# Optimization experiments

Hardware: AMD Instinct MI355X
Metric: run time of the kernel (lower is better)

## Reference

```python
import jax, jax.numpy as jnp
import numpy as np

N = 30000      # nodes
E = 480000     # edges (before self-loops)
F_IN = 128     # dim_in
H = 8          # heads
C = 32         # dim_h (per-head channels)
F_H = H * C    # concat hidden width = 256
NEG_SLOPE = 0.2


def setup_inputs() -> dict:
    key = jax.random.key(0)
    ks = jax.random.split(key, 12)
    def glorot(k, shape, fan):
        return jax.random.normal(k, shape, jnp.float32) * (1.0 / np.sqrt(fan))
    return {
        "x": jax.random.normal(ks[0], (N, F_IN), jnp.float32),
        "edge_index": jax.random.randint(ks[1], (2, E), 0, N),
        "W1": glorot(ks[2], (F_IN, F_H), F_IN),
        "a1_src": glorot(ks[3], (H, C), C),
        "a1_dst": glorot(ks[4], (H, C), C),
        "b1": jnp.zeros((F_H,), jnp.float32),
        "W2": glorot(ks[5], (F_H, F_H), F_H),
        "a2_src": glorot(ks[6], (H, C), C),
        "a2_dst": glorot(ks[7], (H, C), C),
        "b2": jnp.zeros((F_H,), jnp.float32),
        "Wl": glorot(ks[8], (F_H, 1), F_H),
        "bl": jnp.zeros((1,), jnp.float32),
    }


def gat_conv(x, src, dst, W, a_src, a_dst, b):
    """PyG-style GATConv (concat=True, add_self_loops handled by caller)."""
    n = x.shape[0]
    h = (x @ W).reshape(n, H, C)                       # [N,H,C]
    alpha_s = jnp.einsum('nhc,hc->nh', h, a_src)        # [N,H]
    alpha_d = jnp.einsum('nhc,hc->nh', h, a_dst)        # [N,H]
    e = jax.nn.leaky_relu(alpha_s[src] + alpha_d[dst], NEG_SLOPE)  # [E,H]
    # segment softmax over incoming edges of each destination node
    e_max = jax.ops.segment_max(e, dst, num_segments=n)            # [N,H]
    e_max = jnp.where(jnp.isfinite(e_max), e_max, 0.0)
    e_exp = jnp.exp(e - e_max[dst])                                # [E,H]
    denom = jax.ops.segment_sum(e_exp, dst, num_segments=n)        # [N,H]
    alpha = e_exp / (denom[dst] + 1e-16)                           # [E,H]
    out = jax.ops.segment_sum(h[src] * alpha[:, :, None], dst, num_segments=n)  # [N,H,C]
    return out.reshape(n, F_H) + b


def reference(x, edge_index, W1, a1_src, a1_dst, b1, W2, a2_src, a2_dst, b2, Wl, bl):
    loops = jnp.arange(N, dtype=edge_index.dtype)      # self-loops (PyG default)
    src = jnp.concatenate([edge_index[0], loops])
    dst = jnp.concatenate([edge_index[1], loops])
    h = jax.nn.elu(gat_conv(x, src, dst, W1, a1_src, a1_dst, b1))
    h = jax.nn.elu(gat_conv(h, src, dst, W2, a2_src, a2_dst, b2))
    return (h @ Wl + bl).squeeze(1)                    # [N]
```

## Files before the change

kernel.cpp:

```cpp
#include <hip/hip_runtime.h>
#include <hip/hip_bf16.h>

#define NNODES 30000
#define NEDGES 480000
#define TE (NEDGES + NNODES)
#define FH 256
#define NH 8
#define NSB ((NNODES + 255) / 256)

typedef unsigned short ushort_t;
typedef __attribute__((ext_vector_type(8))) _Float16 f16x8;
typedef __attribute__((ext_vector_type(2))) _Float16 f16x2;
typedef __attribute__((ext_vector_type(4))) float f32x4;

__global__ void zero_counts(int* __restrict__ c) {
    int i = blockIdx.x * 256 + threadIdx.x;
    if (i < NNODES) c[i] = 0;
}

__global__ void count_kernel(const int* __restrict__ ei, int* __restrict__ counts) {
    int e = blockIdx.x * 256 + threadIdx.x;
    if (e >= TE) return;
    int d = (e < NEDGES) ? ei[NEDGES + e] : (e - NEDGES);
    atomicAdd(&counts[d], 1);
}

__global__ __launch_bounds__(256) void scan1_kernel(const int* __restrict__ counts,
                                                    int* __restrict__ rp,
                                                    int* __restrict__ bsum) {
    __shared__ int s[256];
    const int tid = threadIdx.x;
    const int i = blockIdx.x * 256 + tid;
    int v = (i < NNODES) ? counts[i] : 0;
    s[tid] = v;
    __syncthreads();
    for (int off = 1; off < 256; off <<= 1) {
        int t = (tid >= off) ? s[tid - off] : 0;
        __syncthreads();
        s[tid] += t;
        __syncthreads();
    }
    if (i < NNODES) rp[i] = s[tid] - v;
    if (tid == 255) bsum[blockIdx.x] = s[255];
}

__global__ __launch_bounds__(128) void scan2_kernel(int* __restrict__ bsum) {
    __shared__ int s[128];
    const int tid = threadIdx.x;
    int v = (tid < NSB) ? bsum[tid] : 0;
    s[tid] = v;
    __syncthreads();
    for (int off = 1; off < 128; off <<= 1) {
        int t = (tid >= off) ? s[tid - off] : 0;
        __syncthreads();
        s[tid] += t;
        __syncthreads();
    }
    if (tid < NSB) bsum[tid] = s[tid] - v;
}

__global__ __launch_bounds__(256) void scan3_kernel(int* __restrict__ rp,
                                                    const int* __restrict__ bsum,
                                                    int* __restrict__ cursor) {
    const int i = blockIdx.x * 256 + threadIdx.x;
    if (i < NNODES) {
        int r = rp[i] + bsum[blockIdx.x];
        rp[i] = r;
        cursor[i] = r;
    }
    if (i == 0) rp[NNODES] = TE;
}

__global__ void fill_kernel(const int* __restrict__ ei, int* __restrict__ cursor,
                            int* __restrict__ ssrc) {
    int e = blockIdx.x * 256 + threadIdx.x;
    if (e >= TE) return;
    int s, d;
    if (e < NEDGES) { s = ei[e]; d = ei[NEDGES + e]; }
    else            { s = e - NEDGES; d = s; }
    int pos = atomicAdd(&cursor[d], 1);
    ssrc[pos] = s;
}

__device__ __forceinline__ unsigned f2h2(float a, float b) {
    f16x2 h;
    h.x = (_Float16)a;
    h.y = (_Float16)b;
    return __builtin_bit_cast(unsigned, h);
}

__global__ void cvtT_w_both(const float* __restrict__ W1, const float* __restrict__ W2,
                            _Float16* __restrict__ t1, _Float16* __restrict__ t2) {
    int idx = blockIdx.x * 256 + threadIdx.x;
    if (idx < 128 * 256) {
        int n = idx & 255, k = idx >> 8;
        t1[n * 128 + k] = (_Float16)W1[idx];
    }
    int j = idx - 128 * 256;
    if (j >= 0 && j < 256 * 256) {
        int n = j & 255, k = j >> 8;
        t2[n * 256 + k] = (_Float16)W2[j];
    }
}

template<int K, bool CVT>
__global__ __launch_bounds__(512) void gemm_mfma(
    const void* __restrict__ Araw,  const _Float16* __restrict__ Bt,
    const float* __restrict__ ASRC, const float* __restrict__ ADST,
    _Float16* __restrict__ HFh, float* __restrict__ AS, float* __restrict__ AD) {

    constexpr int LDK = 40;
    __shared__ _Float16 Ah[128][LDK];
    __shared__ _Float16 Bh[256][LDK];

    const int tid  = threadIdx.x;
    const int lane = tid & 63;
    const int wid  = tid >> 6;
    const int m0 = blockIdx.x * 128;
    const int wm = (wid & 1) * 64;
    const int wn = (wid >> 1) * 64;
    const int q = lane >> 4;
    const int c = lane & 15;

    f32x4 acc[4][4];
#pragma unroll
    for (int mi = 0; mi < 4; ++mi)
#pragma unroll
        for (int ni = 0; ni < 4; ++ni) acc[mi][ni] = (f32x4){0.f, 0.f, 0.f, 0.f};

    for (int k0 = 0; k0 < K; k0 += 32) {
        __syncthreads();
        {
            int row = tid >> 2;
            int ch  = (tid & 3) * 8;
            int gr = m0 + row;
            uint4 v = make_uint4(0u, 0u, 0u, 0u);
            if (gr < NNODES) {
                if (CVT) {
                    const float* Xf = (const float*)Araw;
                    float4 f0 = *reinterpret_cast<const float4*>(&Xf[(size_t)gr * K + k0 + ch]);
                    float4 f1 = *reinterpret_cast<const float4*>(&Xf[(size_t)gr * K + k0 + ch + 4]);
                    v.x = f2h2(f0.x, f0.y); v.y = f2h2(f0.z, f0.w);
                    v.z = f2h2(f1.x, f1.y); v.w = f2h2(f1.z, f1.w);
                } else {
                    const _Float16* Ah_g = (const _Float16*)Araw;
                    v = *reinterpret_cast<const uint4*>(&Ah_g[(size_t)gr * K + k0 + ch]);
                }
            }
            *reinterpret_cast<uint4*>(&Ah[row][ch]) = v;
        }
#pragma unroll
        for (int rep = 0; rep < 2; ++rep) {
            int idx = tid + 512 * rep;
            int row = idx >> 2;
            int ch  = (idx & 3) * 8;
            uint4 bv = *reinterpret_cast<const uint4*>(&Bt[(size_t)row * K + k0 + ch]);
            *reinterpret_cast<uint4*>(&Bh[row][ch]) = bv;
        }
        __syncthreads();

        const int koff = q * 8;
        f16x8 fa[4], fb[4];
#pragma unroll
        for (int mi = 0; mi < 4; ++mi)
            fa[mi] = *reinterpret_cast<const f16x8*>(&Ah[wm + mi * 16 + c][koff]);
#pragma unroll
        for (int ni = 0; ni < 4; ++ni)
            fb[ni] = *reinterpret_cast<const f16x8*>(&Bh[wn + ni * 16 + c][koff]);
#pragma unroll
        for (int mi = 0; mi < 4; ++mi)
#pragma unroll
            for (int ni = 0; ni < 4; ++ni)
                acc[mi][ni] = __builtin_amdgcn_mfma_f32_16x16x32_f16(fa[mi], fb[ni], acc[mi][ni], 0, 0, 0);
    }

    float as_v[4], ad_v[4];
#pragma unroll
    for (int ni = 0; ni < 4; ++ni) {
        as_v[ni] = ASRC[wn + ni * 16 + c];
        ad_v[ni] = ADST[wn + ni * 16 + c];
    }
    const int head0 = wn >> 5;

#pragma unroll
    for (int mi = 0; mi < 4; ++mi) {
#pragma unroll
        for (int j = 0; j < 4; ++j) {
            int row = m0 + wm + mi * 16 + q * 4 + j;
            bool ok = row < NNODES;
            if (ok) {
#pragma unroll
                for (int ni = 0; ni < 4; ++ni)
                    HFh[(size_t)row * FH + wn + ni * 16 + c] = (_Float16)acc[mi][ni][j];
            }
            float ps0 = acc[mi][0][j] * as_v[0] + acc[mi][1][j] * as_v[1];
            float ps1 = acc[mi][2][j] * as_v[2] + acc[mi][3][j] * as_v[3];
            float pd0 = acc[mi][0][j] * ad_v[0] + acc[mi][1][j] * ad_v[1];
            float pd1 = acc[mi][2][j] * ad_v[2] + acc[mi][3][j] * ad_v[3];
#pragma unroll
            for (int off = 8; off >= 1; off >>= 1) {
                ps0 += __shfl_xor(ps0, off);
                ps1 += __shfl_xor(ps1, off);
                pd0 += __shfl_xor(pd0, off);
                pd1 += __shfl_xor(pd1, off);
            }
            if (ok && c == 0) {
                AS[row * NH + head0]     = ps0;
                AS[row * NH + head0 + 1] = ps1;
                AD[row * NH + head0]     = pd0;
                AD[row * NH + head0 + 1] = pd1;
            }
        }
    }
}

template<bool FINAL>
__global__ __launch_bounds__(256) void aggregate(
    const _Float16* __restrict__ HFh,
    const float* __restrict__ AS, const float* __restrict__ AD,
    const int* __restrict__ rp, const int* __restrict__ ssrc,
    const float* __restrict__ BIAS,
    _Float16* __restrict__ X2H,
    const float* __restrict__ WL, const float* __restrict__ BL,
    float* __restrict__ OUT) {

    __shared__ float wslab[4][64 * 10];

    const int tid  = threadIdx.x;
    const int lane = tid & 63;
    const int wid  = tid >> 6;
    const int node = __builtin_amdgcn_readfirstlane(blockIdx.x * 4 + wid);
    const int epar = lane >> 5;
    const int cg   = lane & 31;
    const int hh   = cg >> 2;
    const int c8   = cg * 8;
    float* wl = wslab[wid];

    const int p0  = rp[node];
    const int deg = rp[node + 1] - p0;

    const float4 ad0 = *reinterpret_cast<const float4*>(&AD[node * NH]);
    const float4 ad1 = *reinterpret_cast<const float4*>(&AD[node * NH + 4]);

    float a0=0.f,a1=0.f,a2=0.f,a3=0.f,a4=0.f,a5=0.f,a6=0.f,a7=0.f;
    float den = 0.f;

    for (int base = 0; base < deg; base += 64) {
        const int ne = min(64, deg - base);

        if (lane < ne) {
            int s = ssrc[p0 + base + lane];
            float4 as0 = *reinterpret_cast<const float4*>(&AS[s * NH]);
            float4 as1 = *reinterpret_cast<const float4*>(&AS[s * NH + 4]);
            float sv[8] = {as0.x + ad0.x, as0.y + ad0.y, as0.z + ad0.z, as0.w + ad0.w,
                           as1.x + ad1.x, as1.y + ad1.y, as1.z + ad1.z, as1.w + ad1.w};
            float* wp = &wl[lane * 10];
#pragma unroll
            for (int h = 0; h < 8; ++h) {
                float t = sv[h] > 0.f ? sv[h] : 0.2f * sv[h];
                wp[h] = __expf(t);
            }
            wp[8] = __int_as_float(s);
        }
        asm volatile("s_waitcnt lgkmcnt(0)" ::: "memory");

#pragma unroll 4
        for (int e0 = 0; e0 < ne; e0 += 2) {
            const int  e   = e0 + epar;
            const bool act = e < ne;
            const int  ee  = act ? e : 0;
            const int  sa  = __float_as_int(wl[ee * 10 + 8]);
            const float wr = wl[ee * 10 + hh];
            const float w  = act ? wr : 0.f;
            den += w;
            const f16x8 hv = *reinterpret_cast<const f16x8*>(&HFh[(size_t)sa * FH + c8]);
            a0 = fmaf((float)hv[0], w, a0);
            a1 = fmaf((float)hv[1], w, a1);
            a2 = fmaf((float)hv[2], w, a2);
            a3 = fmaf((float)hv[3], w, a3);
            a4 = fmaf((float)hv[4], w, a4);
            a5 = fmaf((float)hv[5], w, a5);
            a6 = fmaf((float)hv[6], w, a6);
            a7 = fmaf((float)hv[7], w, a7);
        }
    }

    a0 += __shfl_xor(a0, 32); a1 += __shfl_xor(a1, 32);
    a2 += __shfl_xor(a2, 32); a3 += __shfl_xor(a3, 32);
    a4 += __shfl_xor(a4, 32); a5 += __shfl_xor(a5, 32);
    a6 += __shfl_xor(a6, 32); a7 += __shfl_xor(a7, 32);
    den += __shfl_xor(den, 32);

    const float inv = 1.f / (den + 1e-16f);
    const float4 b0 = *reinterpret_cast<const float4*>(&BIAS[c8]);
    const float4 b1 = *reinterpret_cast<const float4*>(&BIAS[c8 + 4]);
    float o[8];
    o[0] = fmaf(a0, inv, b0.x); o[1] = fmaf(a1, inv, b0.y);
    o[2] = fmaf(a2, inv, b0.z); o[3] = fmaf(a3, inv, b0.w);
    o[4] = fmaf(a4, inv, b1.x); o[5] = fmaf(a5, inv, b1.y);
    o[6] = fmaf(a6, inv, b1.z); o[7] = fmaf(a7, inv, b1.w);
#pragma unroll
    for (int j = 0; j < 8; ++j) o[j] = o[j] > 0.f ? o[j] : expm1f(o[j]);

    if (!FINAL) {
        uint2 st;
        st.x = f2h2(o[epar * 4 + 0], o[epar * 4 + 1]);
        st.y = f2h2(o[epar * 4 + 2], o[epar * 4 + 3]);
        *reinterpret_cast<uint2*>(&X2H[(size_t)node * FH + c8 + epar * 4]) = st;
    } else {
        const float4 w0 = *reinterpret_cast<const float4*>(&WL[c8]);
        const float4 w1 = *reinterpret_cast<const float4*>(&WL[c8 + 4]);
        float pl = fmaf(o[0], w0.x, fmaf(o[1], w0.y, fmaf(o[2], w0.z, o[3] * w0.w)));
        pl = fmaf(o[4], w1.x, fmaf(o[5], w1.y, fmaf(o[6], w1.z, fmaf(o[7], w1.w, pl))));
#pragma unroll
        for (int off = 16; off >= 1; off >>= 1) pl += __shfl_xor(pl, off);
        if (lane == 0) OUT[node] = pl + BL[0];
    }
}

extern "C" void kernel_launch(void* const* d_in, const int* in_sizes, int n_in,
                              void* d_out, int out_size, void* d_ws, size_t ws_size,
                              hipStream_t stream) {
    const float* x   = (const float*)d_in[0];
    const int*   ei  = (const int*)d_in[1];
    const float* W1  = (const float*)d_in[2];
    const float* a1s = (const float*)d_in[3];
    const float* a1d = (const float*)d_in[4];
    const float* b1  = (const float*)d_in[5];
    const float* W2  = (const float*)d_in[6];
    const float* a2s = (const float*)d_in[7];
    const float* a2d = (const float*)d_in[8];
    const float* b2  = (const float*)d_in[9];
    const float* Wl  = (const float*)d_in[10];
    const float* bl  = (const float*)d_in[11];
    float* out = (float*)d_out;

    char* w = (char*)d_ws;
    auto alloc = [&](size_t bytes) -> char* {
        char* p = w;
        w += (bytes + 255) & ~size_t(255);
        return p;
    };
    int*   counts = (int*)alloc((size_t)NNODES * 4);
    int*   rp     = (int*)alloc((size_t)(NNODES + 1) * 4);
    int*   cursor = (int*)alloc((size_t)NNODES * 4);
    int*   bsum   = (int*)alloc((size_t)NSB * 4);
    int*   ssrc   = (int*)alloc((size_t)TE * 4);
    _Float16* hfh = (_Float16*)alloc((size_t)NNODES * FH * 2);
    _Float16* x2h = (_Float16*)alloc((size_t)NNODES * FH * 2);
    float* asb    = (float*)alloc((size_t)NNODES * NH * 4);
    float* adb    = (float*)alloc((size_t)NNODES * NH * 4);
    _Float16* w1t = (_Float16*)alloc((size_t)128 * 256 * 2);
    _Float16* w2t = (_Float16*)alloc((size_t)256 * 256 * 2);

    zero_counts<<<NSB, 256, 0, stream>>>(counts);
    count_kernel<<<(TE + 255) / 256, 256, 0, stream>>>(ei, counts);
    scan1_kernel<<<NSB, 256, 0, stream>>>(counts, rp, bsum);
    scan2_kernel<<<1, 128, 0, stream>>>(bsum);
    scan3_kernel<<<NSB, 256, 0, stream>>>(rp, bsum, cursor);
    fill_kernel<<<(TE + 255) / 256, 256, 0, stream>>>(ei, cursor, ssrc);

    cvtT_w_both<<<(128 * 256 + 256 * 256 + 255) / 256, 256, 0, stream>>>(W1, W2, w1t, w2t);

    const int gblocks = (NNODES + 127) / 128;
    gemm_mfma<128, true><<<gblocks, 512, 0, stream>>>(x, w1t, a1s, a1d, hfh, asb, adb);
    aggregate<false><<<NNODES / 4, 256, 0, stream>>>(hfh, asb, adb, rp, ssrc, b1,
                                                     x2h, nullptr, nullptr, nullptr);
    gemm_mfma<256, false><<<gblocks, 512, 0, stream>>>(x2h, w2t, a2s, a2d, hfh, asb, adb);
    aggregate<true><<<NNODES / 4, 256, 0, stream>>>(hfh, asb, adb, rp, ssrc, b2,
                                                    nullptr, Wl, bl, out);
}
```

Before: 179.5 us.

## Fuse CSR build into one persistent kernel with software grid barriers

Replaces the six CSR-construction launches (zero, count, three scan stages, fill) and the weight conversion launch with two kernels. A prep kernel zeroes counts and barrier counters and transposes the weights, and a persistent 120-block CSR kernel performs count, scan and fill, separated by atomic spin grid barriers. This is meant to remove launch overhead and inter-kernel gaps, in exchange for relying on all 120 blocks being co-resident and running the count and fill phases on far fewer threads.

```diff
diff --git a/kernel.cpp b/kernel.cpp
--- a/kernel.cpp
+++ b/kernel.cpp
@@ -6,81 +6,13 @@
 #define TE (NEDGES + NNODES)
 #define FH 256
 #define NH 8
-#define NSB ((NNODES + 255) / 256)
+#define CSRB 120
+#define CHUNK 250
 
 typedef unsigned short ushort_t;
 typedef __attribute__((ext_vector_type(8))) _Float16 f16x8;
 typedef __attribute__((ext_vector_type(2))) _Float16 f16x2;
 typedef __attribute__((ext_vector_type(4))) float f32x4;
-
-__global__ void zero_counts(int* __restrict__ c) {
-    int i = blockIdx.x * 256 + threadIdx.x;
-    if (i < NNODES) c[i] = 0;
-}
-
-__global__ void count_kernel(const int* __restrict__ ei, int* __restrict__ counts) {
-    int e = blockIdx.x * 256 + threadIdx.x;
-    if (e >= TE) return;
-    int d = (e < NEDGES) ? ei[NEDGES + e] : (e - NEDGES);
-    atomicAdd(&counts[d], 1);
-}
-
-__global__ __launch_bounds__(256) void scan1_kernel(const int* __restrict__ counts,
-                                                    int* __restrict__ rp,
-                                                    int* __restrict__ bsum) {
-    __shared__ int s[256];
-    const int tid = threadIdx.x;
-    const int i = blockIdx.x * 256 + tid;
-    int v = (i < NNODES) ? counts[i] : 0;
-    s[tid] = v;
-    __syncthreads();
-    for (int off = 1; off < 256; off <<= 1) {
-        int t = (tid >= off) ? s[tid - off] : 0;
-        __syncthreads();
-        s[tid] += t;
-        __syncthreads();
-    }
-    if (i < NNODES) rp[i] = s[tid] - v;
-    if (tid == 255) bsum[blockIdx.x] = s[255];
-}
-
-__global__ __launch_bounds__(128) void scan2_kernel(int* __restrict__ bsum) {
-    __shared__ int s[128];
-    const int tid = threadIdx.x;
-    int v = (tid < NSB) ? bsum[tid] : 0;
-    s[tid] = v;
-    __syncthreads();
-    for (int off = 1; off < 128; off <<= 1) {
-        int t = (tid >= off) ? s[tid - off] : 0;
-        __syncthreads();
-        s[tid] += t;
-        __syncthreads();
-    }
-    if (tid < NSB) bsum[tid] = s[tid] - v;
-}
-
-__global__ __launch_bounds__(256) void scan3_kernel(int* __restrict__ rp,
-                                                    const int* __restrict__ bsum,
-                                                    int* __restrict__ cursor) {
-    const int i = blockIdx.x * 256 + threadIdx.x;
-    if (i < NNODES) {
-        int r = rp[i] + bsum[blockIdx.x];
-        rp[i] = r;
-        cursor[i] = r;
-    }
-    if (i == 0) rp[NNODES] = TE;
-}
-
-__global__ void fill_kernel(const int* __restrict__ ei, int* __restrict__ cursor,
-                            int* __restrict__ ssrc) {
-    int e = blockIdx.x * 256 + threadIdx.x;
-    if (e >= TE) return;
-    int s, d;
-    if (e < NEDGES) { s = ei[e]; d = ei[NEDGES + e]; }
-    else            { s = e - NEDGES; d = s; }
-    int pos = atomicAdd(&cursor[d], 1);
-    ssrc[pos] = s;
-}
 
 __device__ __forceinline__ unsigned f2h2(float a, float b) {
     f16x2 h;
@@ -89,17 +21,94 @@
     return __builtin_bit_cast(unsigned, h);
 }
 
-__global__ void cvtT_w_both(const float* __restrict__ W1, const float* __restrict__ W2,
-                            _Float16* __restrict__ t1, _Float16* __restrict__ t2) {
-    int idx = blockIdx.x * 256 + threadIdx.x;
-    if (idx < 128 * 256) {
-        int n = idx & 255, k = idx >> 8;
-        t1[n * 128 + k] = (_Float16)W1[idx];
-    }
-    int j = idx - 128 * 256;
+__global__ __launch_bounds__(256) void prep_kernel(
+    int* __restrict__ counts, int* __restrict__ bar,
+    const float* __restrict__ W1, const float* __restrict__ W2,
+    _Float16* __restrict__ t1, _Float16* __restrict__ t2) {
+    int i = blockIdx.x * 256 + threadIdx.x;
+    if (i < NNODES) counts[i] = 0;
+    if (i < 8) bar[i] = 0;
+    if (i < 128 * 256) {
+        int n = i & 255, k = i >> 8;
+        t1[n * 128 + k] = (_Float16)W1[i];
+    }
+    int j = i - 128 * 256;
     if (j >= 0 && j < 256 * 256) {
         int n = j & 255, k = j >> 8;
         t2[n * 256 + k] = (_Float16)W2[j];
+    }
+}
+
+__device__ __forceinline__ void gridbar(int* __restrict__ bar, int phase, int tid) {
+    __syncthreads();
+    if (tid == 0) {
+        __threadfence();
+        atomicAdd(&bar[phase], 1);
+        while (__hip_atomic_load(&bar[phase], __ATOMIC_ACQUIRE,
+                                 __HIP_MEMORY_SCOPE_AGENT) < CSRB) { }
+    }
+    __syncthreads();
+}
+
+__global__ __launch_bounds__(256) void csr_kernel(
+    const int* __restrict__ ei, int* __restrict__ counts,
+    int* __restrict__ rp, int* __restrict__ cursor, int* __restrict__ ssrc,
+    int* __restrict__ bar, int* __restrict__ bsum) {
+
+    __shared__ int s[256];
+    const int tid  = threadIdx.x;
+    const int bid  = blockIdx.x;
+    const int gtid = bid * 256 + tid;
+    const int gsz  = CSRB * 256;
+
+    for (int e = gtid; e < TE; e += gsz) {
+        int d = (e < NEDGES) ? ei[NEDGES + e] : (e - NEDGES);
+        atomicAdd(&counts[d], 1);
+    }
+    gridbar(bar, 0, tid);
+
+    const int base = bid * CHUNK;
+    int v = (tid < CHUNK) ? counts[base + tid] : 0;
+    s[tid] = v;
+    __syncthreads();
+    for (int off = 1; off < 256; off <<= 1) {
+        int t = (tid >= off) ? s[tid - off] : 0;
+        __syncthreads();
+        s[tid] += t;
+        __syncthreads();
+    }
+    if (tid < CHUNK) rp[base + tid] = s[tid] - v;
+    if (tid == 255) bsum[bid] = s[255];
+    gridbar(bar, 1, tid);
+
+    if (bid == 0) {
+        int vv = (tid < CSRB) ? bsum[tid] : 0;
+        s[tid] = vv;
+        __syncthreads();
+        for (int off = 1; off < 256; off <<= 1) {
+            int t = (tid >= off) ? s[tid - off] : 0;
+            __syncthreads();
+            s[tid] += t;
+            __syncthreads();
+        }
+        if (tid < CSRB) bsum[tid] = s[tid] - vv;
+    }
+    gridbar(bar, 2, tid);
+
+    if (tid < CHUNK) {
+        int r = rp[base + tid] + bsum[bid];
+        rp[base + tid] = r;
+        cursor[base + tid] = r;
+    }
+    if (gtid == 0) rp[NNODES] = TE;
+    gridbar(bar, 3, tid);
+
+    for (int e = gtid; e < TE; e += gsz) {
+        int sv, d;
+        if (e < NEDGES) { sv = ei[e]; d = ei[NEDGES + e]; }
+        else            { sv = e - NEDGES; d = sv; }
+        int pos = atomicAdd(&cursor[d], 1);
+        ssrc[pos] = sv;
     }
 }
 
@@ -344,7 +353,8 @@
     int*   counts = (int*)alloc((size_t)NNODES * 4);
     int*   rp     = (int*)alloc((size_t)(NNODES + 1) * 4);
     int*   cursor = (int*)alloc((size_t)NNODES * 4);
-    int*   bsum   = (int*)alloc((size_t)NSB * 4);
+    int*   bar    = (int*)alloc(8 * 4);
+    int*   bsum   = (int*)alloc((size_t)CSRB * 4);
     int*   ssrc   = (int*)alloc((size_t)TE * 4);
     _Float16* hfh = (_Float16*)alloc((size_t)NNODES * FH * 2);
     _Float16* x2h = (_Float16*)alloc((size_t)NNODES * FH * 2);
@@ -353,14 +363,8 @@
     _Float16* w1t = (_Float16*)alloc((size_t)128 * 256 * 2);
     _Float16* w2t = (_Float16*)alloc((size_t)256 * 256 * 2);
 
-    zero_counts<<<NSB, 256, 0, stream>>>(counts);
-    count_kernel<<<(TE + 255) / 256, 256, 0, stream>>>(ei, counts);
-    scan1_kernel<<<NSB, 256, 0, stream>>>(counts, rp, bsum);
-    scan2_kernel<<<1, 128, 0, stream>>>(bsum);
-    scan3_kernel<<<NSB, 256, 0, stream>>>(rp, bsum, cursor);
-    fill_kernel<<<(TE + 255) / 256, 256, 0, stream>>>(ei, cursor, ssrc);
-
-    cvtT_w_both<<<(128 * 256 + 256 * 256 + 255) / 256, 256, 0, stream>>>(W1, W2, w1t, w2t);
+    prep_kernel<<<384, 256, 0, stream>>>(counts, bar, W1, W2, w1t, w2t);
+    csr_kernel<<<CSRB, 256, 0, stream>>>(ei, counts, rp, cursor, ssrc, bar, bsum);
 
     const int gblocks = (NNODES + 127) / 128;
     gemm_mfma<128, true><<<gblocks, 512, 0, stream>>>(x, w1t, a1s, a1d, hfh, asb, adb);
```

Result: slower. 197.5 us (+10.0%).

## Fuse CSR build launches: merge prep, overlap counting with GEMM, single-pass scan

Applied to the files above, without the earlier changes.

Merges zero-count and weight conversion into one prep kernel. Folds edge counting into extra blocks of the first GEMM launch so the two run concurrently. Replaces the three-kernel scan with a single-pass scan where each block publishes its sum through flagged 64-bit atomics and later blocks spin on them. The goal is fewer launches and less serialized time; the spin-wait relies on earlier blocks being scheduled first, which could deadlock if that ordering does not hold.

```diff
diff --git a/kernel.cpp b/kernel.cpp
--- a/kernel.cpp
+++ b/kernel.cpp
@@ -7,30 +7,48 @@
 #define FH 256
 #define NH 8
 #define NSB ((NNODES + 255) / 256)
+#define CNTB 235
 
 typedef unsigned short ushort_t;
 typedef __attribute__((ext_vector_type(8))) _Float16 f16x8;
 typedef __attribute__((ext_vector_type(2))) _Float16 f16x2;
 typedef __attribute__((ext_vector_type(4))) float f32x4;
 
-__global__ void zero_counts(int* __restrict__ c) {
+__device__ __forceinline__ unsigned f2h2(float a, float b) {
+    f16x2 h;
+    h.x = (_Float16)a;
+    h.y = (_Float16)b;
+    return __builtin_bit_cast(unsigned, h);
+}
+
+__global__ __launch_bounds__(256) void prep_kernel(
+    int* __restrict__ counts, unsigned long long* __restrict__ pub,
+    const float* __restrict__ W1, const float* __restrict__ W2,
+    _Float16* __restrict__ t1, _Float16* __restrict__ t2) {
     int i = blockIdx.x * 256 + threadIdx.x;
-    if (i < NNODES) c[i] = 0;
-}
-
-__global__ void count_kernel(const int* __restrict__ ei, int* __restrict__ counts) {
-    int e = blockIdx.x * 256 + threadIdx.x;
-    if (e >= TE) return;
-    int d = (e < NEDGES) ? ei[NEDGES + e] : (e - NEDGES);
-    atomicAdd(&counts[d], 1);
-}
-
-__global__ __launch_bounds__(256) void scan1_kernel(const int* __restrict__ counts,
-                                                    int* __restrict__ rp,
-                                                    int* __restrict__ bsum) {
+    if (i < NNODES) counts[i] = 0;
+    if (i < NSB) pub[i] = 0ULL;
+    if (i < 128 * 256) {
+        int n = i & 255, k = i >> 8;
+        t1[n * 128 + k] = (_Float16)W1[i];
+    }
+    int j = i - 128 * 256;
+    if (j >= 0 && j < 256 * 256) {
+        int n = j & 255, k = j >> 8;
+        t2[n * 256 + k] = (_Float16)W2[j];
+    }
+}
+
+__global__ __launch_bounds__(256) void scan_lb(
+    const int* __restrict__ counts, int* __restrict__ rp,
+    int* __restrict__ cursor, unsigned long long* __restrict__ pub) {
+
     __shared__ int s[256];
+    __shared__ int ppart[128];
     const int tid = threadIdx.x;
-    const int i = blockIdx.x * 256 + tid;
+    const int bid = blockIdx.x;
+    const int i = bid * 256 + tid;
+
     int v = (i < NNODES) ? counts[i] : 0;
     s[tid] = v;
     __syncthreads();
@@ -40,40 +58,41 @@
         s[tid] += t;
         __syncthreads();
     }
-    if (i < NNODES) rp[i] = s[tid] - v;
-    if (tid == 255) bsum[blockIdx.x] = s[255];
-}
-
-__global__ __launch_bounds__(128) void scan2_kernel(int* __restrict__ bsum) {
-    __shared__ int s[128];
-    const int tid = threadIdx.x;
-    int v = (tid < NSB) ? bsum[tid] : 0;
-    s[tid] = v;
+    if (tid == 255)
+        __hip_atomic_store(&pub[bid], (1ULL << 63) | (unsigned)s[255],
+                           __ATOMIC_RELEASE, __HIP_MEMORY_SCOPE_AGENT);
+
+    if (tid < 128) {
+        int total = 0;
+        if (tid < bid) {
+            unsigned long long val;
+            do {
+                val = __hip_atomic_load(&pub[tid], __ATOMIC_ACQUIRE,
+                                        __HIP_MEMORY_SCOPE_AGENT);
+            } while (!(val >> 63));
+            total = (int)(unsigned)val;
+        }
+        ppart[tid] = total;
+    }
     __syncthreads();
-    for (int off = 1; off < 128; off <<= 1) {
-        int t = (tid >= off) ? s[tid - off] : 0;
-        __syncthreads();
-        s[tid] += t;
-        __syncthreads();
-    }
-    if (tid < NSB) bsum[tid] = s[tid] - v;
-}
-
-__global__ __launch_bounds__(256) void scan3_kernel(int* __restrict__ rp,
-                                                    const int* __restrict__ bsum,
-                                                    int* __restrict__ cursor) {
-    const int i = blockIdx.x * 256 + threadIdx.x;
+    for (int off = 64; off >= 1; off >>= 1) {
+        if (tid < off) ppart[tid] += ppart[tid + off];
+        __syncthreads();
+    }
+    const int boff = ppart[0];
+
     if (i < NNODES) {
-        int r = rp[i] + bsum[blockIdx.x];
+        int r = boff + s[tid] - v;
         rp[i] = r;
         cursor[i] = r;
     }
     if (i == 0) rp[NNODES] = TE;
 }
 
-__global__ void fill_kernel(const int* __restrict__ ei, int* __restrict__ cursor,
-                            int* __restrict__ ssrc) {
-    int e = blockIdx.x * 256 + threadIdx.x;
+__global__ __launch_bounds__(512) void fill_kernel(const int* __restrict__ ei,
+                                                   int* __restrict__ cursor,
+                                                   int* __restrict__ ssrc) {
+    int e = blockIdx.x * 512 + threadIdx.x;
     if (e >= TE) return;
     int s, d;
     if (e < NEDGES) { s = ei[e]; d = ei[NEDGES + e]; }
@@ -82,38 +101,28 @@
     ssrc[pos] = s;
 }
 
-__device__ __forceinline__ unsigned f2h2(float a, float b) {
-    f16x2 h;
-    h.x = (_Float16)a;
-    h.y = (_Float16)b;
-    return __builtin_bit_cast(unsigned, h);
-}
-
-__global__ void cvtT_w_both(const float* __restrict__ W1, const float* __restrict__ W2,
-                            _Float16* __restrict__ t1, _Float16* __restrict__ t2) {
-    int idx = blockIdx.x * 256 + threadIdx.x;
-    if (idx < 128 * 256) {
-        int n = idx & 255, k = idx >> 8;
-        t1[n * 128 + k] = (_Float16)W1[idx];
-    }
-    int j = idx - 128 * 256;
-    if (j >= 0 && j < 256 * 256) {
-        int n = j & 255, k = j >> 8;
-        t2[n * 256 + k] = (_Float16)W2[j];
-    }
-}
-
 template<int K, bool CVT>
 __global__ __launch_bounds__(512) void gemm_mfma(
     const void* __restrict__ Araw,  const _Float16* __restrict__ Bt,
     const float* __restrict__ ASRC, const float* __restrict__ ADST,
-    _Float16* __restrict__ HFh, float* __restrict__ AS, float* __restrict__ AD) {
+    _Float16* __restrict__ HFh, float* __restrict__ AS, float* __restrict__ AD,
+    int gb, const int* __restrict__ ei, int* __restrict__ counts) {
 
     constexpr int LDK = 40;
     __shared__ _Float16 Ah[128][LDK];
     __shared__ _Float16 Bh[256][LDK];
 
     const int tid  = threadIdx.x;
+
+    if ((int)blockIdx.x >= gb) {
+        const int cb = blockIdx.x - gb;
+        for (int e = cb * 512 + tid; e < TE; e += CNTB * 512) {
+            int d = (e < NEDGES) ? ei[NEDGES + e] : (e - NEDGES);
+            atomicAdd(&counts[d], 1);
+        }
+        return;
+    }
+
     const int lane = tid & 63;
     const int wid  = tid >> 6;
     const int m0 = blockIdx.x * 128;
@@ -344,7 +353,7 @@
     int*   counts = (int*)alloc((size_t)NNODES * 4);
     int*   rp     = (int*)alloc((size_t)(NNODES + 1) * 4);
     int*   cursor = (int*)alloc((size_t)NNODES * 4);
-    int*   bsum   = (int*)alloc((size_t)NSB * 4);
+    unsigned long long* pub = (unsigned long long*)alloc((size_t)NSB * 8);
     int*   ssrc   = (int*)alloc((size_t)TE * 4);
     _Float16* hfh = (_Float16*)alloc((size_t)NNODES * FH * 2);
     _Float16* x2h = (_Float16*)alloc((size_t)NNODES * FH * 2);
@@ -353,20 +362,17 @@
     _Float16* w1t = (_Float16*)alloc((size_t)128 * 256 * 2);
     _Float16* w2t = (_Float16*)alloc((size_t)256 * 256 * 2);
 
-    zero_counts<<<NSB, 256, 0, stream>>>(counts);
-    count_kernel<<<(TE + 255) / 256, 256, 0, stream>>>(ei, counts);
-    scan1_kernel<<<NSB, 256, 0, stream>>>(counts, rp, bsum);
-    scan2_kernel<<<1, 128, 0, stream>>>(bsum);
-    scan3_kernel<<<NSB, 256, 0, stream>>>(rp, bsum, cursor);
-    fill_kernel<<<(TE + 255) / 256, 256, 0, stream>>>(ei, cursor, ssrc);
-
-    cvtT_w_both<<<(128 * 256 + 256 * 256 + 255) / 256, 256, 0, stream>>>(W1, W2, w1t, w2t);
-
     const int gblocks = (NNODES + 127) / 128;
-    gemm_mfma<128, true><<<gblocks, 512, 0, stream>>>(x, w1t, a1s, a1d, hfh, asb, adb);
+
+    prep_kernel<<<384, 256, 0, stream>>>(counts, pub, W1, W2, w1t, w2t);
+    gemm_mfma<128, true><<<gblocks + CNTB, 512, 0, stream>>>(
+        x, w1t, a1s, a1d, hfh, asb, adb, gblocks, ei, counts);
+    scan_lb<<<NSB, 256, 0, stream>>>(counts, rp, cursor, pub);
+    fill_kernel<<<(TE + 511) / 512, 512, 0, stream>>>(ei, cursor, ssrc);
     aggregate<false><<<NNODES / 4, 256, 0, stream>>>(hfh, asb, adb, rp, ssrc, b1,
                                                      x2h, nullptr, nullptr, nullptr);
-    gemm_mfma<256, false><<<gblocks, 512, 0, stream>>>(x2h, w2t, a2s, a2d, hfh, asb, adb);
+    gemm_mfma<256, false><<<gblocks, 512, 0, stream>>>(
+        x2h, w2t, a2s, a2d, hfh, asb, adb, gblocks, nullptr, nullptr);
     aggregate<true><<<NNODES / 4, 256, 0, stream>>>(hfh, asb, adb, rp, ssrc, b2,
                                                     nullptr, Wl, bl, out);
 }
```

Measured after the change: 172.0 us. -4.2%, faster.
